# Kernel tuning notes

Hardware: AMD Instinct MI355X
Metric: run time of the kernel (lower is better)

The kernel has to match this reference:

```python
import jax, jax.numpy as jnp
import numpy as np

EPS = 1e-5  # torch BatchNorm default eps
B_SEG = 64
PTS_PER_SEG = 16384
N_TOTAL = B_SEG * PTS_PER_SEG
D_IN = 32
D_OUT = 64


def setup_inputs() -> dict:
    key = jax.random.key(0)
    k = jax.random.split(key, 4)
    x = jax.random.normal(k[0], (N_TOTAL, D_IN), dtype=jnp.float32)
    length = jnp.full((B_SEG,), PTS_PER_SEG, dtype=jnp.int32)
    # conv1d_1: Conv1d(32, 1, 1) -> weight [1,32,1], bias [1]; flatten to vector/scalar
    w1 = jax.random.normal(k[1], (D_IN,), dtype=jnp.float32) * 0.1
    b1 = jnp.zeros((), dtype=jnp.float32)
    # bn_1: BatchNorm1d(1)
    g1 = jnp.ones((), dtype=jnp.float32)
    beta1 = jnp.zeros((), dtype=jnp.float32)
    # fc_1: Linear(32, 64)
    W2 = jax.random.normal(k[2], (D_IN, D_OUT), dtype=jnp.float32) * 0.05
    b2 = jnp.zeros((D_OUT,), dtype=jnp.float32)
    # bn_2: BatchNorm1d(64)
    g2 = jnp.ones((D_OUT,), dtype=jnp.float32)
    beta2 = jnp.zeros((D_OUT,), dtype=jnp.float32)
    return {"x": x, "length": length, "w1": w1, "b1": b1, "g1": g1,
            "beta1": beta1, "W2": W2, "b2": b2, "g2": g2, "beta2": beta2}


def reference(x, length, w1, b1, g1, beta1, W2, b2, g2, beta2):
    N = x.shape[0]
    B = length.shape[0]
    # conv1d(32->1, k=1) over all N points: per-point scalar score
    z = x @ w1 + b1                                        # [N]
    # BatchNorm1d(1) in training mode: stats over all N points (biased var)
    mu = jnp.mean(z)
    var = jnp.var(z)
    out1 = g1 * (z - mu) * jax.lax.rsqrt(var + EPS) + beta1  # [N]

    # segment ids from ragged lengths (total length is static)
    seg = jnp.repeat(jnp.arange(B, dtype=jnp.int32), length,
                     total_repeat_length=N)                 # [N]

    # sft = mean(x * out1[:,None], axis=1), softmax per segment
    s = jnp.mean(x * out1[:, None], axis=1)                 # [N]
    smax = jax.ops.segment_max(s, seg, num_segments=B)      # [B]
    e = jnp.exp(s - smax[seg])                              # [N]
    denom = jax.ops.segment_sum(e, seg, num_segments=B)     # [B]
    w = e / denom[seg]                                      # [N] softmax weights

    # temp = mean over segment of (x * w)  (mean, not weighted sum)
    pooled = jax.ops.segment_sum(x * w[:, None], seg, num_segments=B)
    pooled = pooled / length[:, None].astype(x.dtype)       # [B, 32]

    # fc + BatchNorm1d(64) in training mode (stats over B rows)
    h = pooled @ W2 + b2                                    # [B, 64]
    mu2 = jnp.mean(h, axis=0)
    var2 = jnp.var(h, axis=0)
    out = g2 * (h - mu2) * jax.lax.rsqrt(var2 + EPS) + beta2
    return out
```

## Files before the change

kernel.cpp:

```cpp
#include <hip/hip_runtime.h>


#define EPS 1e-5f
#define NSB 2048

#define WS_DPART   0
#define WS_CONSTS  32768
#define WS_OFFS    32800
#define WS_GNUM    33280
#define WS_GDEN    41472
#define WS_ZERO_OFF 33280
#define WS_ZERO_SZ  8448

__global__ __launch_bounds__(256) void k_stats(const float* __restrict__ x,
                                               const float* __restrict__ w1,
                                               const float* __restrict__ b1,
                                               int N, int rpb,
                                               double* __restrict__ dpart) {
    const int tid = threadIdx.x;
    const int q = tid & 7;
    const float4 w4 = ((const float4*)w1)[q];
    const float b1v = b1[0];
    const float4* __restrict__ xv = (const float4*)x;
    const int row0 = blockIdx.x * rpb;
    const int iters = (rpb + 31) >> 5;

    double accZ = 0.0, accZZ = 0.0;
    for (int it = 0; it < iters; ++it) {
        int row = row0 + it * 32 + (tid >> 3);
        if (row < N) {
            float4 v = xv[row * 8 + q];
            float zp = v.x * w4.x + v.y * w4.y + v.z * w4.z + v.w * w4.w;
            zp += __shfl_xor(zp, 1);
            zp += __shfl_xor(zp, 2);
            zp += __shfl_xor(zp, 4);
            if (q == 0) {
                float z = zp + b1v;
                accZ  += (double)z;
                accZZ += (double)z * (double)z;
            }
        }
    }

    __shared__ double sZ[256], sZZ[256];
    sZ[tid] = accZ; sZZ[tid] = accZZ;
    __syncthreads();
    for (int s = 128; s > 0; s >>= 1) {
        if (tid < s) { sZ[tid] += sZ[tid + s]; sZZ[tid] += sZZ[tid + s]; }
        __syncthreads();
    }
    if (tid == 0) {
        dpart[2 * blockIdx.x]     = sZ[0];
        dpart[2 * blockIdx.x + 1] = sZZ[0];
    }
}

__global__ __launch_bounds__(256) void k_consts(const double* __restrict__ dpart,
                                                const int* __restrict__ length,
                                                const float* __restrict__ g1,
                                                const float* __restrict__ beta1,
                                                int N, int B,
                                                float* __restrict__ consts,
                                                int* __restrict__ offs) {
    __shared__ double sZ[256], sZZ[256];
    const int tid = threadIdx.x;
    double aZ = 0.0, aZZ = 0.0;
    for (int i = tid; i < NSB; i += 256) {
        aZ  += dpart[2 * i];
        aZZ += dpart[2 * i + 1];
    }
    sZ[tid] = aZ; sZZ[tid] = aZZ;
    __syncthreads();
    for (int s = 128; s > 0; s >>= 1) {
        if (tid < s) { sZ[tid] += sZ[tid + s]; sZZ[tid] += sZZ[tid + s]; }
        __syncthreads();
    }
    if (tid == 0) {
        double mu  = sZ[0] / (double)N;
        double var = sZZ[0] / (double)N - mu * mu;
        float c1 = (float)((double)g1[0] / sqrt(var + (double)EPS));
        float c2 = beta1[0] - (float)(c1 * mu);
        consts[0] = c1;
        consts[1] = c2;
        int o = 0;
        offs[0] = 0;
        for (int b = 0; b < B; ++b) { o += length[b]; offs[b + 1] = o; }
    }
}

__global__ __launch_bounds__(256) void k_pool(const float* __restrict__ x,
                                              const float* __restrict__ w1,
                                              const float* __restrict__ b1,
                                              const float* __restrict__ consts,
                                              const int* __restrict__ offs,
                                              float* __restrict__ gnum,
                                              float* __restrict__ gden) {
    const int tid = threadIdx.x;
    const int q = tid & 7;
    const int b = blockIdx.y;
    const int off = offs[b];
    const int len = offs[b + 1] - off;
    const int nch = gridDim.x;
    const int rpc = (len + nch - 1) / nch;
    const int r0 = blockIdx.x * rpc;
    const int r1 = min(r0 + rpc, len);

    const float4 w4 = ((const float4*)w1)[q];
    const float b1v = b1[0];
    const float c1 = consts[0], c2 = consts[1];
    const float4* __restrict__ xv = (const float4*)x;

    float4 acc = make_float4(0.f, 0.f, 0.f, 0.f);
    float accE = 0.f;

    for (int r = r0 + (tid >> 3); r < r1; r += 32) {
        int row = off + r;
        float4 v = xv[row * 8 + q];
        float zp = v.x * w4.x + v.y * w4.y + v.z * w4.z + v.w * w4.w;
        float rp = v.x + v.y + v.z + v.w;
        zp += __shfl_xor(zp, 1);  rp += __shfl_xor(rp, 1);
        zp += __shfl_xor(zp, 2);  rp += __shfl_xor(rp, 2);
        zp += __shfl_xor(zp, 4);  rp += __shfl_xor(rp, 4);
        float z = zp + b1v;
        float s = (c1 * z + c2) * rp * 0.03125f;
        float e = __expf(s);
        acc.x += e * v.x; acc.y += e * v.y; acc.z += e * v.z; acc.w += e * v.w;
        if (q == 0) accE += e;
    }

    for (int m = 8; m <= 32; m <<= 1) {
        acc.x += __shfl_xor(acc.x, m);
        acc.y += __shfl_xor(acc.y, m);
        acc.z += __shfl_xor(acc.z, m);
        acc.w += __shfl_xor(acc.w, m);
        accE  += __shfl_xor(accE, m);
    }
    const int lane = tid & 63;
    if (lane < 8) {
        atomicAdd(&gnum[b * 32 + lane * 4 + 0], acc.x);
        atomicAdd(&gnum[b * 32 + lane * 4 + 1], acc.y);
        atomicAdd(&gnum[b * 32 + lane * 4 + 2], acc.z);
        atomicAdd(&gnum[b * 32 + lane * 4 + 3], acc.w);
        if (lane == 0) atomicAdd(&gden[b], accE);
    }
}

__global__ __launch_bounds__(256) void k_head(const float* __restrict__ gnum,
                                              const float* __restrict__ gden,
                                              const int* __restrict__ length,
                                              const float* __restrict__ W2,
                                              const float* __restrict__ b2,
                                              const float* __restrict__ g2,
                                              const float* __restrict__ beta2,
                                              float* __restrict__ out, int B) {
    __shared__ float pooled[64 * 32];
    __shared__ float h[64 * 64];
    __shared__ float mu2[64], isd[64];
    const int tid = threadIdx.x;

    for (int i = tid; i < B * 32; i += 256) {
        int bb = i >> 5;
        pooled[i] = gnum[i] / (gden[bb] * (float)length[bb]);
    }
    __syncthreads();

    const int j = tid & 63;
    const int g = tid >> 6;
    for (int r = 0; r < 16; ++r) {
        int bb = g * 16 + r;
        if (bb < B) {
            float hv = b2[j];
            for (int k = 0; k < 32; ++k) hv += pooled[bb * 32 + k] * W2[k * 64 + j];
            h[bb * 64 + j] = hv;
        }
    }
    __syncthreads();

    if (tid < 64) {
        float m = 0.f;
        for (int bb = 0; bb < B; ++bb) m += h[bb * 64 + tid];
        m /= (float)B;
        float v = 0.f;
        for (int bb = 0; bb < B; ++bb) { float d = h[bb * 64 + tid] - m; v += d * d; }
        v /= (float)B;
        mu2[tid] = m;
        isd[tid] = rsqrtf(v + EPS);
    }
    __syncthreads();

    for (int r = 0; r < 16; ++r) {
        int bb = g * 16 + r;
        if (bb < B) {
            int idx = bb * 64 + j;
            out[idx] = g2[j] * (h[idx] - mu2[j]) * isd[j] + beta2[j];
        }
    }
}

extern "C" void kernel_launch(void* const* d_in, const int* in_sizes, int n_in,
                              void* d_out, int out_size, void* d_ws, size_t ws_size,
                              hipStream_t stream) {
    const float* x      = (const float*)d_in[0];
    const int*   length = (const int*)  d_in[1];
    const float* w1     = (const float*)d_in[2];
    const float* b1     = (const float*)d_in[3];
    const float* g1     = (const float*)d_in[4];
    const float* beta1  = (const float*)d_in[5];
    const float* W2     = (const float*)d_in[6];
    const float* b2     = (const float*)d_in[7];
    const float* g2     = (const float*)d_in[8];
    const float* beta2  = (const float*)d_in[9];
    float* out = (float*)d_out;

    const int N = in_sizes[0] / 32;
    const int B = in_sizes[1];

    char* ws = (char*)d_ws;
    double* dpart  = (double*)(ws + WS_DPART);
    float*  consts = (float*) (ws + WS_CONSTS);
    int*    offs   = (int*)   (ws + WS_OFFS);
    float*  gnum   = (float*) (ws + WS_GNUM);
    float*  gden   = (float*) (ws + WS_GDEN);

    hipMemsetAsync(ws + WS_ZERO_OFF, 0, WS_ZERO_SZ, stream);

    int rpb = (N + NSB - 1) / NSB;
    rpb = (rpb + 31) & ~31;

    k_stats <<<NSB, 256, 0, stream>>>(x, w1, b1, N, rpb, dpart);
    k_consts<<<1,   256, 0, stream>>>(dpart, length, g1, beta1, N, B, consts, offs);
    k_pool  <<<dim3(32, B), 256, 0, stream>>>(x, w1, b1, consts, offs, gnum, gden);
    k_head  <<<1,   256, 0, stream>>>(gnum, gden, length, W2, b2, g2, beta2, out, B);
}
```

Baseline: 298.7 us.

## Switch stats and pool kernels to one row per thread

Both streaming kernels now give each thread a whole 128-byte row instead of splitting a row across 8 lanes with shuffle reductions. The dot product and row sum become plain per-thread FMAs, and the per-row shuffles disappear. The pool kernel keeps 32 float accumulators per thread, which raises register pressure and needs a bigger final wave reduction. Loads become strided per lane, which may hurt coalescing. The memset is also dropped and the accumulators are zeroed in k_consts instead.

```diff
diff --git a/kernel.cpp b/kernel.cpp
--- a/kernel.cpp
+++ b/kernel.cpp
@@ -9,37 +9,32 @@
 #define WS_OFFS    32800
 #define WS_GNUM    33280
 #define WS_GDEN    41472
-#define WS_ZERO_OFF 33280
-#define WS_ZERO_SZ  8448
 
 __global__ __launch_bounds__(256) void k_stats(const float* __restrict__ x,
                                                const float* __restrict__ w1,
                                                const float* __restrict__ b1,
-                                               int N, int rpb,
+                                               int N,
                                                double* __restrict__ dpart) {
     const int tid = threadIdx.x;
-    const int q = tid & 7;
-    const float4 w4 = ((const float4*)w1)[q];
     const float b1v = b1[0];
     const float4* __restrict__ xv = (const float4*)x;
-    const int row0 = blockIdx.x * rpb;
-    const int iters = (rpb + 31) >> 5;
-
+
+    const int stride = gridDim.x * 256;
     double accZ = 0.0, accZZ = 0.0;
-    for (int it = 0; it < iters; ++it) {
-        int row = row0 + it * 32 + (tid >> 3);
-        if (row < N) {
-            float4 v = xv[row * 8 + q];
-            float zp = v.x * w4.x + v.y * w4.y + v.z * w4.z + v.w * w4.w;
-            zp += __shfl_xor(zp, 1);
-            zp += __shfl_xor(zp, 2);
-            zp += __shfl_xor(zp, 4);
-            if (q == 0) {
-                float z = zp + b1v;
-                accZ  += (double)z;
-                accZZ += (double)z * (double)z;
-            }
-        }
+
+    for (int row = blockIdx.x * 256 + tid; row < N; row += stride) {
+        const float4* __restrict__ rp = xv + (size_t)row * 8;
+        float z = b1v;
+#pragma unroll
+        for (int i = 0; i < 8; ++i) {
+            float4 v = rp[i];
+            z = fmaf(v.x, w1[4 * i + 0], z);
+            z = fmaf(v.y, w1[4 * i + 1], z);
+            z = fmaf(v.z, w1[4 * i + 2], z);
+            z = fmaf(v.w, w1[4 * i + 3], z);
+        }
+        accZ  += (double)z;
+        accZZ += (double)z * (double)z;
     }
 
     __shared__ double sZ[256], sZZ[256];
@@ -61,9 +56,15 @@
                                                 const float* __restrict__ beta1,
                                                 int N, int B,
                                                 float* __restrict__ consts,
-                                                int* __restrict__ offs) {
+                                                int* __restrict__ offs,
+                                                float* __restrict__ gnum,
+                                                float* __restrict__ gden) {
     __shared__ double sZ[256], sZZ[256];
     const int tid = threadIdx.x;
+
+    for (int i = tid; i < B * 32; i += 256) gnum[i] = 0.f;
+    if (tid < B) gden[tid] = 0.f;
+
     double aZ = 0.0, aZZ = 0.0;
     for (int i = tid; i < NSB; i += 256) {
         aZ  += dpart[2 * i];
@@ -96,7 +97,6 @@
                                               float* __restrict__ gnum,
                                               float* __restrict__ gden) {
     const int tid = threadIdx.x;
-    const int q = tid & 7;
     const int b = blockIdx.y;
     const int off = offs[b];
     const int len = offs[b + 1] - off;
@@ -105,42 +105,58 @@
     const int r0 = blockIdx.x * rpc;
     const int r1 = min(r0 + rpc, len);
 
-    const float4 w4 = ((const float4*)w1)[q];
     const float b1v = b1[0];
     const float c1 = consts[0], c2 = consts[1];
     const float4* __restrict__ xv = (const float4*)x;
 
-    float4 acc = make_float4(0.f, 0.f, 0.f, 0.f);
+    float4 acc[8];
+#pragma unroll
+    for (int i = 0; i < 8; ++i) acc[i] = make_float4(0.f, 0.f, 0.f, 0.f);
     float accE = 0.f;
 
-    for (int r = r0 + (tid >> 3); r < r1; r += 32) {
-        int row = off + r;
-        float4 v = xv[row * 8 + q];
-        float zp = v.x * w4.x + v.y * w4.y + v.z * w4.z + v.w * w4.w;
-        float rp = v.x + v.y + v.z + v.w;
-        zp += __shfl_xor(zp, 1);  rp += __shfl_xor(rp, 1);
-        zp += __shfl_xor(zp, 2);  rp += __shfl_xor(rp, 2);
-        zp += __shfl_xor(zp, 4);  rp += __shfl_xor(rp, 4);
-        float z = zp + b1v;
-        float s = (c1 * z + c2) * rp * 0.03125f;
+    for (int r = r0 + tid; r < r1; r += 256) {
+        const float4* __restrict__ rp = xv + (size_t)(off + r) * 8;
+        float4 v[8];
+#pragma unroll
+        for (int i = 0; i < 8; ++i) v[i] = rp[i];
+        float z = b1v, m = 0.f;
+#pragma unroll
+        for (int i = 0; i < 8; ++i) {
+            z = fmaf(v[i].x, w1[4 * i + 0], z);
+            z = fmaf(v[i].y, w1[4 * i + 1], z);
+            z = fmaf(v[i].z, w1[4 * i + 2], z);
+            z = fmaf(v[i].w, w1[4 * i + 3], z);
+            m += v[i].x + v[i].y + v[i].z + v[i].w;
+        }
+        float s = (c1 * z + c2) * m * 0.03125f;
         float e = __expf(s);
-        acc.x += e * v.x; acc.y += e * v.y; acc.z += e * v.z; acc.w += e * v.w;
-        if (q == 0) accE += e;
-    }
-
-    for (int m = 8; m <= 32; m <<= 1) {
-        acc.x += __shfl_xor(acc.x, m);
-        acc.y += __shfl_xor(acc.y, m);
-        acc.z += __shfl_xor(acc.z, m);
-        acc.w += __shfl_xor(acc.w, m);
-        accE  += __shfl_xor(accE, m);
+#pragma unroll
+        for (int i = 0; i < 8; ++i) {
+            acc[i].x = fmaf(e, v[i].x, acc[i].x);
+            acc[i].y = fmaf(e, v[i].y, acc[i].y);
+            acc[i].z = fmaf(e, v[i].z, acc[i].z);
+            acc[i].w = fmaf(e, v[i].w, acc[i].w);
+        }
+        accE += e;
+    }
+
+#pragma unroll
+    for (int msk = 1; msk < 64; msk <<= 1) {
+#pragma unroll
+        for (int i = 0; i < 8; ++i) {
+            acc[i].x += __shfl_xor(acc[i].x, msk);
+            acc[i].y += __shfl_xor(acc[i].y, msk);
+            acc[i].z += __shfl_xor(acc[i].z, msk);
+            acc[i].w += __shfl_xor(acc[i].w, msk);
+        }
+        accE += __shfl_xor(accE, msk);
     }
     const int lane = tid & 63;
     if (lane < 8) {
-        atomicAdd(&gnum[b * 32 + lane * 4 + 0], acc.x);
-        atomicAdd(&gnum[b * 32 + lane * 4 + 1], acc.y);
-        atomicAdd(&gnum[b * 32 + lane * 4 + 2], acc.z);
-        atomicAdd(&gnum[b * 32 + lane * 4 + 3], acc.w);
+        atomicAdd(&gnum[b * 32 + lane * 4 + 0], acc[lane].x);
+        atomicAdd(&gnum[b * 32 + lane * 4 + 1], acc[lane].y);
+        atomicAdd(&gnum[b * 32 + lane * 4 + 2], acc[lane].z);
+        atomicAdd(&gnum[b * 32 + lane * 4 + 3], acc[lane].w);
         if (lane == 0) atomicAdd(&gden[b], accE);
     }
 }
@@ -222,13 +238,9 @@
     float*  gnum   = (float*) (ws + WS_GNUM);
     float*  gden   = (float*) (ws + WS_GDEN);
 
-    hipMemsetAsync(ws + WS_ZERO_OFF, 0, WS_ZERO_SZ, stream);
-
-    int rpb = (N + NSB - 1) / NSB;
-    rpb = (rpb + 31) & ~31;
-
-    k_stats <<<NSB, 256, 0, stream>>>(x, w1, b1, N, rpb, dpart);
-    k_consts<<<1,   256, 0, stream>>>(dpart, length, g1, beta1, N, B, consts, offs);
+    k_stats <<<NSB, 256, 0, stream>>>(x, w1, b1, N, dpart);
+    k_consts<<<1,   256, 0, stream>>>(dpart, length, g1, beta1, N, B,
+                                      consts, offs, gnum, gden);
     k_pool  <<<dim3(32, B), 256, 0, stream>>>(x, w1, b1, consts, offs, gnum, gden);
     k_head  <<<1,   256, 0, stream>>>(gnum, gden, length, W2, b2, g2, beta2, out, B);
 }
```

Result: slower. 307.2 us (+2.8%).

## Pipeline x loads through LDS via async global_load_lds in stats and pool kernels

Applied to the files above, without the earlier changes.

Both streaming kernels now give each wave a contiguous row range and prefetch rows several stages ahead into a per-wave LDS ring using global_load_lds, waiting on vmcnt before reading each stage. The stats kernel swaps its shared-memory tree reduction for wave shuffles, and the pool kernel combines the per-wave partials in LDS so each block issues 33 atomics instead of 33 per wave. The memset is dropped and the accumulators are zeroed inside k_consts instead. The aim is to keep more memory requests in flight on a bandwidth-bound pass over x, at the cost of tricky hand-written waitcnt logic that depends on exactly how the compiler orders loads.

```diff
diff --git a/kernel.cpp b/kernel.cpp
--- a/kernel.cpp
+++ b/kernel.cpp
@@ -3,55 +3,89 @@
 
 #define EPS 1e-5f
 #define NSB 2048
+#define CHUNKS 32
+#define PIPE 3
+#define RING 4
 
 #define WS_DPART   0
 #define WS_CONSTS  32768
 #define WS_OFFS    32800
 #define WS_GNUM    33280
 #define WS_GDEN    41472
-#define WS_ZERO_OFF 33280
-#define WS_ZERO_SZ  8448
-
-__global__ __launch_bounds__(256) void k_stats(const float* __restrict__ x,
-                                               const float* __restrict__ w1,
-                                               const float* __restrict__ b1,
-                                               int N, int rpb,
-                                               double* __restrict__ dpart) {
+
+__device__ __forceinline__ void ldsdma16(const void* g, void* l) {
+    __builtin_amdgcn_global_load_lds(
+        (const __attribute__((address_space(1))) void*)g,
+        (__attribute__((address_space(3))) void*)l, 16, 0, 0);
+}
+
+__device__ __forceinline__ void wait_stage(int rem) {
+    if (rem >= 2)      asm volatile("s_waitcnt vmcnt(2)" ::: "memory");
+    else if (rem == 1) asm volatile("s_waitcnt vmcnt(1)" ::: "memory");
+    else               asm volatile("s_waitcnt vmcnt(0)" ::: "memory");
+}
+
+__global__ __launch_bounds__(256, 8) void k_stats(const float* __restrict__ x,
+                                                  const float* __restrict__ w1,
+                                                  const float* __restrict__ b1,
+                                                  int N,
+                                                  double* __restrict__ dpart) {
+    __shared__ float4 ring[4][RING][64];
+    __shared__ double sdz[4], sdzz[4];
     const int tid = threadIdx.x;
-    const int q = tid & 7;
+    const int w = tid >> 6, lane = tid & 63;
+    const int q = lane & 7;
+
     const float4 w4 = ((const float4*)w1)[q];
     const float b1v = b1[0];
+    asm volatile("s_waitcnt vmcnt(0)" ::: "memory");
+
     const float4* __restrict__ xv = (const float4*)x;
-    const int row0 = blockIdx.x * rpb;
-    const int iters = (rpb + 31) >> 5;
+    const int Nm1 = N - 1;
+    const int rpb = (N + NSB - 1) / NSB;
+    const int wpr = (rpb + 3) >> 2;
+    const int br0 = blockIdx.x * rpb;
+    const int wr0 = br0 + w * wpr;
+    const int wend = min(min(wr0 + wpr, br0 + rpb), N);
+    const int span = wend - wr0;
+    const int nst = (span + 7) >> 3;
 
     double accZ = 0.0, accZZ = 0.0;
-    for (int it = 0; it < iters; ++it) {
-        int row = row0 + it * 32 + (tid >> 3);
-        if (row < N) {
-            float4 v = xv[row * 8 + q];
+
+    if (span > 0) {
+        for (int p = 0; p < PIPE && p < nst; ++p) {
+            int row = min(wr0 + p * 8 + (lane >> 3), Nm1);
+            ldsdma16(xv + (size_t)row * 8 + q, &ring[w][p & (RING - 1)][0]);
+        }
+        for (int st = 0; st < nst; ++st) {
+            wait_stage(nst - 1 - st < PIPE - 1 ? nst - 1 - st : PIPE - 1);
+            float4 v = ring[w][st & (RING - 1)][lane];
+            asm volatile("" ::: "memory");
+            if (st + PIPE < nst) {
+                int row = min(wr0 + (st + PIPE) * 8 + (lane >> 3), Nm1);
+                ldsdma16(xv + (size_t)row * 8 + q,
+                         &ring[w][(st + PIPE) & (RING - 1)][0]);
+            }
             float zp = v.x * w4.x + v.y * w4.y + v.z * w4.z + v.w * w4.w;
             zp += __shfl_xor(zp, 1);
             zp += __shfl_xor(zp, 2);
             zp += __shfl_xor(zp, 4);
-            if (q == 0) {
-                float z = zp + b1v;
-                accZ  += (double)z;
-                accZZ += (double)z * (double)z;
-            }
-        }
-    }
-
-    __shared__ double sZ[256], sZZ[256];
-    sZ[tid] = accZ; sZZ[tid] = accZZ;
-    __syncthreads();
-    for (int s = 128; s > 0; s >>= 1) {
-        if (tid < s) { sZ[tid] += sZ[tid + s]; sZZ[tid] += sZZ[tid + s]; }
-        __syncthreads();
-    }
+            int row = wr0 + st * 8 + (lane >> 3);
+            float z = (row < wend) ? (zp + b1v) : 0.f;
+            accZ  += (double)z;
+            accZZ += (double)z * (double)z;
+        }
+    }
+#pragma unroll
+    for (int m = 8; m <= 32; m <<= 1) {
+        accZ  += __shfl_xor(accZ, m);
+        accZZ += __shfl_xor(accZZ, m);
+    }
+    if (lane == 0) { sdz[w] = accZ; sdzz[w] = accZZ; }
+    __syncthreads();
     if (tid == 0) {
-        dpart[2 * blockIdx.x]     = sZ[0];
-        dpart[2 * blockIdx.x + 1] = sZZ[0];
+        dpart[2 * blockIdx.x]     = sdz[0] + sdz[1] + sdz[2] + sdz[3];
+        dpart[2 * blockIdx.x + 1] = sdzz[0] + sdzz[1] + sdzz[2] + sdzz[3];
     }
 }
 
@@ -61,9 +95,15 @@
                                                 const float* __restrict__ beta1,
                                                 int N, int B,
                                                 float* __restrict__ consts,
-                                                int* __restrict__ offs) {
+                                                int* __restrict__ offs,
+                                                float* __restrict__ gnum,
+                                                float* __restrict__ gden) {
     __shared__ double sZ[256], sZZ[256];
     const int tid = threadIdx.x;
+
+    for (int i = tid; i < B * 32; i += 256) gnum[i] = 0.f;
+    if (tid < B) gden[tid] = 0.f;
+
     double aZ = 0.0, aZZ = 0.0;
     for (int i = tid; i < NSB; i += 256) {
         aZ  += dpart[2 * i];
@@ -79,55 +119,83 @@
         double mu  = sZ[0] / (double)N;
         double var = sZZ[0] / (double)N - mu * mu;
         float c1 = (float)((double)g1[0] / sqrt(var + (double)EPS));
-        float c2 = beta1[0] - (float)(c1 * mu);
         consts[0] = c1;
-        consts[1] = c2;
+        consts[1] = beta1[0] - (float)(c1 * mu);
         int o = 0;
         offs[0] = 0;
         for (int b = 0; b < B; ++b) { o += length[b]; offs[b + 1] = o; }
     }
 }
 
-__global__ __launch_bounds__(256) void k_pool(const float* __restrict__ x,
-                                              const float* __restrict__ w1,
-                                              const float* __restrict__ b1,
-                                              const float* __restrict__ consts,
-                                              const int* __restrict__ offs,
-                                              float* __restrict__ gnum,
-                                              float* __restrict__ gden) {
+__global__ __launch_bounds__(256, 8) void k_pool(const float* __restrict__ x,
+                                                 const float* __restrict__ w1,
+                                                 const float* __restrict__ b1,
+                                                 const float* __restrict__ consts,
+                                                 const int* __restrict__ offs,
+                                                 int N,
+                                                 float* __restrict__ gnum,
+                                                 float* __restrict__ gden) {
+    __shared__ float4 ring[4][RING][64];
+    __shared__ float sred[4][33];
     const int tid = threadIdx.x;
-    const int q = tid & 7;
-    const int b = blockIdx.y;
-    const int off = offs[b];
-    const int len = offs[b + 1] - off;
-    const int nch = gridDim.x;
-    const int rpc = (len + nch - 1) / nch;
-    const int r0 = blockIdx.x * rpc;
-    const int r1 = min(r0 + rpc, len);
+    const int w = tid >> 6, lane = tid & 63;
+    const int q = lane & 7;
+    const int c = blockIdx.x, b = blockIdx.y;
 
     const float4 w4 = ((const float4*)w1)[q];
     const float b1v = b1[0];
     const float c1 = consts[0], c2 = consts[1];
+    const int off = offs[b], len = offs[b + 1] - off;
+    asm volatile("s_waitcnt vmcnt(0)" ::: "memory");
+
+    const int rpc = (len + CHUNKS - 1) / CHUNKS;
+    const int r0 = c * rpc;
+    const int r1 = min(r0 + rpc, len);
+    const int wpr = (rpc + 3) >> 2;
+    const int wrel0 = r0 + w * wpr;
+    const int wrel1 = min(wrel0 + wpr, r1);
+    const int span = wrel1 - wrel0;
+    const int nst = (span + 7) >> 3;
+    const int wr0 = off + wrel0;
+    const int wend = off + wrel1;
     const float4* __restrict__ xv = (const float4*)x;
+    const int Nm1 = N - 1;
 
     float4 acc = make_float4(0.f, 0.f, 0.f, 0.f);
     float accE = 0.f;
 
-    for (int r = r0 + (tid >> 3); r < r1; r += 32) {
-        int row = off + r;
-        float4 v = xv[row * 8 + q];
-        float zp = v.x * w4.x + v.y * w4.y + v.z * w4.z + v.w * w4.w;
-        float rp = v.x + v.y + v.z + v.w;
-        zp += __shfl_xor(zp, 1);  rp += __shfl_xor(rp, 1);
-        zp += __shfl_xor(zp, 2);  rp += __shfl_xor(rp, 2);
-        zp += __shfl_xor(zp, 4);  rp += __shfl_xor(rp, 4);
-        float z = zp + b1v;
-        float s = (c1 * z + c2) * rp * 0.03125f;
-        float e = __expf(s);
-        acc.x += e * v.x; acc.y += e * v.y; acc.z += e * v.z; acc.w += e * v.w;
-        if (q == 0) accE += e;
-    }
-
+    if (span > 0) {
+        for (int p = 0; p < PIPE && p < nst; ++p) {
+            int row = min(wr0 + p * 8 + (lane >> 3), Nm1);
+            ldsdma16(xv + (size_t)row * 8 + q, &ring[w][p & (RING - 1)][0]);
+        }
+        for (int st = 0; st < nst; ++st) {
+            wait_stage(nst - 1 - st < PIPE - 1 ? nst - 1 - st : PIPE - 1);
+            float4 v = ring[w][st & (RING - 1)][lane];
+            asm volatile("" ::: "memory");
+            if (st + PIPE < nst) {
+                int row = min(wr0 + (st + PIPE) * 8 + (lane >> 3), Nm1);
+                ldsdma16(xv + (size_t)row * 8 + q,
+                         &ring[w][(st + PIPE) & (RING - 1)][0]);
+            }
+            float zp = v.x * w4.x + v.y * w4.y + v.z * w4.z + v.w * w4.w;
+            float mp = v.x + v.y + v.z + v.w;
+            zp += __shfl_xor(zp, 1);  mp += __shfl_xor(mp, 1);
+            zp += __shfl_xor(zp, 2);  mp += __shfl_xor(mp, 2);
+            zp += __shfl_xor(zp, 4);  mp += __shfl_xor(mp, 4);
+            float z = zp + b1v;
+            float s = (c1 * z + c2) * mp * 0.03125f;
+            float e = __expf(s);
+            int row = wr0 + st * 8 + (lane >> 3);
+            e = (row < wend) ? e : 0.f;
+            acc.x = fmaf(e, v.x, acc.x);
+            acc.y = fmaf(e, v.y, acc.y);
+            acc.z = fmaf(e, v.z, acc.z);
+            acc.w = fmaf(e, v.w, acc.w);
+            accE += e;
+        }
+    }
+#pragma unroll
     for (int m = 8; m <= 32; m <<= 1) {
         acc.x += __shfl_xor(acc.x, m);
         acc.y += __shfl_xor(acc.y, m);
@@ -135,13 +203,18 @@
         acc.w += __shfl_xor(acc.w, m);
         accE  += __shfl_xor(accE, m);
     }
-    const int lane = tid & 63;
     if (lane < 8) {
-        atomicAdd(&gnum[b * 32 + lane * 4 + 0], acc.x);
-        atomicAdd(&gnum[b * 32 + lane * 4 + 1], acc.y);
-        atomicAdd(&gnum[b * 32 + lane * 4 + 2], acc.z);
-        atomicAdd(&gnum[b * 32 + lane * 4 + 3], acc.w);
-        if (lane == 0) atomicAdd(&gden[b], accE);
+        sred[w][4 * lane + 0] = acc.x;
+        sred[w][4 * lane + 1] = acc.y;
+        sred[w][4 * lane + 2] = acc.z;
+        sred[w][4 * lane + 3] = acc.w;
+        if (lane == 0) sred[w][32] = accE;
+    }
+    __syncthreads();
+    if (tid < 33) {
+        float s = sred[0][tid] + sred[1][tid] + sred[2][tid] + sred[3][tid];
+        if (tid < 32) atomicAdd(&gnum[b * 32 + tid], s);
+        else          atomicAdd(&gden[b], s);
     }
 }
 
@@ -222,13 +295,10 @@
     float*  gnum   = (float*) (ws + WS_GNUM);
     float*  gden   = (float*) (ws + WS_GDEN);
 
-    hipMemsetAsync(ws + WS_ZERO_OFF, 0, WS_ZERO_SZ, stream);
-
-    int rpb = (N + NSB - 1) / NSB;
-    rpb = (rpb + 31) & ~31;
-
-    k_stats <<<NSB, 256, 0, stream>>>(x, w1, b1, N, rpb, dpart);
-    k_consts<<<1,   256, 0, stream>>>(dpart, length, g1, beta1, N, B, consts, offs);
-    k_pool  <<<dim3(32, B), 256, 0, stream>>>(x, w1, b1, consts, offs, gnum, gden);
+    k_stats <<<NSB, 256, 0, stream>>>(x, w1, b1, N, dpart);
+    k_consts<<<1,   256, 0, stream>>>(dpart, length, g1, beta1, N, B,
+                                      consts, offs, gnum, gden);
+    k_pool  <<<dim3(CHUNKS, B), 256, 0, stream>>>(x, w1, b1, consts, offs, N,
+                                                  gnum, gden);
     k_head  <<<1,   256, 0, stream>>>(gnum, gden, length, W2, b2, g2, beta2, out, B);
 }
```

New measurement: 257.2 us. 1.16x faster.
